# Kernel tuning notes

Measured on AMD Instinct MI355X. Metric: run time of the kernel, lower is better.

## Reference

```python
import jax, jax.numpy as jnp
import numpy as np


def setup_inputs() -> dict:
    key = jax.random.key(0)
    k1, k2 = jax.random.split(key)
    B, C, H, W = 8, 128, 96, 160
    x1 = jax.random.normal(k1, (B, C, H, W), dtype=jnp.float32)
    x2 = jax.random.normal(k2, (B, C, H, W), dtype=jnp.float32)
    return {"x1": x1, "x2": x2, "d": 4}


def reference(x1, x2, d):
    # x1, x2: (B, C, H, W); output: (B, (2d+1)^2, H, W)
    b, c, h, w = x1.shape
    x2p = jnp.pad(x2, ((0, 0), (0, 0), (d, d), (d, d)))
    # Loop over the small fixed (2d+1)^2 displacement set (81 for d=4);
    # each term is a channel-reduced elementwise product (shift-multiply-sum).
    corrs = [
        jnp.einsum("bchw,bchw->bhw", x1,
                   jax.lax.dynamic_slice(x2p, (0, 0, i, j), (b, c, h, w)))
        for i in range(2 * d + 1)
        for j in range(2 * d + 1)
    ]
    out = jnp.stack(corrs, axis=1)  # (B, (2d+1)^2, H, W)
    return out / c
```

## Files before the change

### kernel.cpp

```cpp
#include <hip/hip_runtime.h>
#include <stdint.h>
#include <stddef.h>

#define Bb 8
#define Cc 128
#define Hh 96
#define Ww 160
#define HW (Hh*Ww)
#define Kk 81

typedef __attribute__((ext_vector_type(8))) short short8;
typedef __attribute__((ext_vector_type(4))) float floatx4;
typedef __attribute__((ext_vector_type(4))) unsigned int uintx4;

__device__ __forceinline__ uint32_t bf16rne(float f) {
  uint32_t u = __float_as_uint(f);
  return (u + 0x7FFFu + ((u >> 16) & 1u)) >> 16;
}


#define TPX 32
__global__ __launch_bounds__(256)
void transpose_kernel(const float* __restrict__ x1, const float* __restrict__ x2,
                      ushort* __restrict__ x1t, ushort* __restrict__ x2t) {
  __shared__ float lds[TPX * 130];
  const int t   = threadIdx.x;
  const int b   = blockIdx.y;
  const int hw0 = blockIdx.x * TPX;
  const float* src = blockIdx.z ? x2 : x1;
  ushort*      dst = blockIdx.z ? x2t : x1t;

  const int p4 = t & 7;
  const int cb = t >> 3;
#pragma unroll
  for (int i = 0; i < 4; ++i) {
    const int c = cb + i * 32;
    floatx4 v = *(const floatx4*)&src[(size_t)(b * Cc + c) * HW + hw0 + p4 * 4];
#pragma unroll
    for (int jj = 0; jj < 4; ++jj)
      lds[(p4 * 4 + jj) * 130 + c] = v[jj];
  }
  __syncthreads();

  const int px = t >> 3;
#pragma unroll
  for (int i = 0; i < 2; ++i) {
    const int k = (t & 7) + 8 * i;
    const float* row = &lds[px * 130 + k * 8];
    uint32_t q0 = bf16rne(row[0]) | (bf16rne(row[1]) << 16);
    uint32_t q1 = bf16rne(row[2]) | (bf16rne(row[3]) << 16);
    uint32_t q2 = bf16rne(row[4]) | (bf16rne(row[5]) << 16);
    uint32_t q3 = bf16rne(row[6]) | (bf16rne(row[7]) << 16);
    *(uintx4*)&dst[((size_t)b * HW + hw0 + px) * Cc + k * 8] = (uintx4){q0, q1, q2, q3};
  }
}

#define LOADA(dst, tt, ckc)                                                    \
  {                                                                            \
    dst = (short8){0, 0, 0, 0, 0, 0, 0, 0};                                    \
    if (okw && (unsigned)(gh2b + (tt)) < (unsigned)Hh)                         \
      dst = *(const short8*)&base2[(long)(tt) * (Ww * Cc) + (ckc) * 32];       \
  }

__global__ __launch_bounds__(256, 3)
void corr_t2_kernel(const ushort* __restrict__ x1t, const ushort* __restrict__ x2t,
                    float* __restrict__ out) {
  const int tid  = threadIdx.x;
  const int flat = blockIdx.x;
  const int b  = flat & 7;
  const int j  = flat >> 3;
  const int by = j / 10;
  const int bx = j - by * 10;
  const int w0 = bx * 16;
  const int h0 = by * 4;

  const int lane = tid & 63;
  const int wv   = tid >> 6;
  const int vy = wv & 1, vx = wv >> 1;
  const int n = lane & 15, quad = lane >> 4;
  const int s = n >> 3, pw = n & 7;

  floatx4 acc[10];
#pragma unroll
  for (int t = 0; t < 10; ++t) acc[t] = (floatx4){0.f, 0.f, 0.f, 0.f};

  const int gw2  = w0 - 4 + 8 * vx + n;
  const bool okw = (unsigned)gw2 < (unsigned)Ww;
  const int gh2b = h0 - 4 + 2 * vy;
  const ushort* base2 = x2t + ((long)b * HW + (long)gh2b * Ww + gw2) * Cc + quad * 8;
  const ushort* base1 = x1t + ((long)b * HW + (long)(h0 + 2 * vy + s) * Ww
                               + (w0 + 8 * vx + pw)) * Cc + quad * 8;

  const short8 bf0 = *(const short8*)&base1[0 * 32];
  const short8 bf1 = *(const short8*)&base1[1 * 32];
  const short8 bf2 = *(const short8*)&base1[2 * 32];
  const short8 bf3 = *(const short8*)&base1[3 * 32];

  short8 aA0, aA1, aA2, aA3, aA4, aA5, aA6, aA7, aA8, aA9;
  short8 aB0, aB1, aB2, aB3, aB4, aB5, aB6, aB7, aB8, aB9;

  LOADA(aA0, 0, 0); LOADA(aA1, 1, 0); LOADA(aA2, 2, 0); LOADA(aA3, 3, 0);
  LOADA(aA4, 4, 0); LOADA(aA5, 5, 0); LOADA(aA6, 6, 0); LOADA(aA7, 7, 0);
  LOADA(aA8, 8, 0); LOADA(aA9, 9, 0);

  LOADA(aB0, 0, 1); LOADA(aB1, 1, 1); LOADA(aB2, 2, 1); LOADA(aB3, 3, 1);
  LOADA(aB4, 4, 1); LOADA(aB5, 5, 1); LOADA(aB6, 6, 1); LOADA(aB7, 7, 1);
  LOADA(aB8, 8, 1); LOADA(aB9, 9, 1);
  acc[0] = __builtin_amdgcn_mfma_f32_16x16x32_bf16(aA0, bf0, acc[0], 0, 0, 0);
  acc[1] = __builtin_amdgcn_mfma_f32_16x16x32_bf16(aA1, bf0, acc[1], 0, 0, 0);
  acc[2] = __builtin_amdgcn_mfma_f32_16x16x32_bf16(aA2, bf0, acc[2], 0, 0, 0);
  acc[3] = __builtin_amdgcn_mfma_f32_16x16x32_bf16(aA3, bf0, acc[3], 0, 0, 0);
  acc[4] = __builtin_amdgcn_mfma_f32_16x16x32_bf16(aA4, bf0, acc[4], 0, 0, 0);
  acc[5] = __builtin_amdgcn_mfma_f32_16x16x32_bf16(aA5, bf0, acc[5], 0, 0, 0);
  acc[6] = __builtin_amdgcn_mfma_f32_16x16x32_bf16(aA6, bf0, acc[6], 0, 0, 0);
  acc[7] = __builtin_amdgcn_mfma_f32_16x16x32_bf16(aA7, bf0, acc[7], 0, 0, 0);
  acc[8] = __builtin_amdgcn_mfma_f32_16x16x32_bf16(aA8, bf0, acc[8], 0, 0, 0);
  acc[9] = __builtin_amdgcn_mfma_f32_16x16x32_bf16(aA9, bf0, acc[9], 0, 0, 0);

  LOADA(aA0, 0, 2); LOADA(aA1, 1, 2); LOADA(aA2, 2, 2); LOADA(aA3, 3, 2);
  LOADA(aA4, 4, 2); LOADA(aA5, 5, 2); LOADA(aA6, 6, 2); LOADA(aA7, 7, 2);
  LOADA(aA8, 8, 2); LOADA(aA9, 9, 2);
  acc[0] = __builtin_amdgcn_mfma_f32_16x16x32_bf16(aB0, bf1, acc[0], 0, 0, 0);
  acc[1] = __builtin_amdgcn_mfma_f32_16x16x32_bf16(aB1, bf1, acc[1], 0, 0, 0);
  acc[2] = __builtin_amdgcn_mfma_f32_16x16x32_bf16(aB2, bf1, acc[2], 0, 0, 0);
  acc[3] = __builtin_amdgcn_mfma_f32_16x16x32_bf16(aB3, bf1, acc[3], 0, 0, 0);
  acc[4] = __builtin_amdgcn_mfma_f32_16x16x32_bf16(aB4, bf1, acc[4], 0, 0, 0);
  acc[5] = __builtin_amdgcn_mfma_f32_16x16x32_bf16(aB5, bf1, acc[5], 0, 0, 0);
  acc[6] = __builtin_amdgcn_mfma_f32_16x16x32_bf16(aB6, bf1, acc[6], 0, 0, 0);
  acc[7] = __builtin_amdgcn_mfma_f32_16x16x32_bf16(aB7, bf1, acc[7], 0, 0, 0);
  acc[8] = __builtin_amdgcn_mfma_f32_16x16x32_bf16(aB8, bf1, acc[8], 0, 0, 0);
  acc[9] = __builtin_amdgcn_mfma_f32_16x16x32_bf16(aB9, bf1, acc[9], 0, 0, 0);

  LOADA(aB0, 0, 3); LOADA(aB1, 1, 3); LOADA(aB2, 2, 3); LOADA(aB3, 3, 3);
  LOADA(aB4, 4, 3); LOADA(aB5, 5, 3); LOADA(aB6, 6, 3); LOADA(aB7, 7, 3);
  LOADA(aB8, 8, 3); LOADA(aB9, 9, 3);
  acc[0] = __builtin_amdgcn_mfma_f32_16x16x32_bf16(aA0, bf2, acc[0], 0, 0, 0);
  acc[1] = __builtin_amdgcn_mfma_f32_16x16x32_bf16(aA1, bf2, acc[1], 0, 0, 0);
  acc[2] = __builtin_amdgcn_mfma_f32_16x16x32_bf16(aA2, bf2, acc[2], 0, 0, 0);
  acc[3] = __builtin_amdgcn_mfma_f32_16x16x32_bf16(aA3, bf2, acc[3], 0, 0, 0);
  acc[4] = __builtin_amdgcn_mfma_f32_16x16x32_bf16(aA4, bf2, acc[4], 0, 0, 0);
  acc[5] = __builtin_amdgcn_mfma_f32_16x16x32_bf16(aA5, bf2, acc[5], 0, 0, 0);
  acc[6] = __builtin_amdgcn_mfma_f32_16x16x32_bf16(aA6, bf2, acc[6], 0, 0, 0);
  acc[7] = __builtin_amdgcn_mfma_f32_16x16x32_bf16(aA7, bf2, acc[7], 0, 0, 0);
  acc[8] = __builtin_amdgcn_mfma_f32_16x16x32_bf16(aA8, bf2, acc[8], 0, 0, 0);
  acc[9] = __builtin_amdgcn_mfma_f32_16x16x32_bf16(aA9, bf2, acc[9], 0, 0, 0);

  acc[0] = __builtin_amdgcn_mfma_f32_16x16x32_bf16(aB0, bf3, acc[0], 0, 0, 0);
  acc[1] = __builtin_amdgcn_mfma_f32_16x16x32_bf16(aB1, bf3, acc[1], 0, 0, 0);
  acc[2] = __builtin_amdgcn_mfma_f32_16x16x32_bf16(aB2, bf3, acc[2], 0, 0, 0);
  acc[3] = __builtin_amdgcn_mfma_f32_16x16x32_bf16(aB3, bf3, acc[3], 0, 0, 0);
  acc[4] = __builtin_amdgcn_mfma_f32_16x16x32_bf16(aB4, bf3, acc[4], 0, 0, 0);
  acc[5] = __builtin_amdgcn_mfma_f32_16x16x32_bf16(aB5, bf3, acc[5], 0, 0, 0);
  acc[6] = __builtin_amdgcn_mfma_f32_16x16x32_bf16(aB6, bf3, acc[6], 0, 0, 0);
  acc[7] = __builtin_amdgcn_mfma_f32_16x16x32_bf16(aB7, bf3, acc[7], 0, 0, 0);
  acc[8] = __builtin_amdgcn_mfma_f32_16x16x32_bf16(aB8, bf3, acc[8], 0, 0, 0);
  acc[9] = __builtin_amdgcn_mfma_f32_16x16x32_bf16(aB9, bf3, acc[9], 0, 0, 0);

  const float scale = 1.0f / 128.0f;
  const int ph  = h0 + 2 * vy + s;
  const int pwg = w0 + 8 * vx + pw;
#pragma unroll
  for (int t = 0; t < 10; ++t) {
    int di = t - 4 - s;
    if ((unsigned)(di + 4) > 8u) continue;
#pragma unroll
    for (int r = 0; r < 4; ++r) {
      int dj = quad * 4 + r - 4 - pw;
      if ((unsigned)(dj + 4) > 8u) continue;
      int kk = (di + 4) * 9 + (dj + 4);
      out[((size_t)b * Kk + kk) * HW + ph * Ww + pwg] = acc[t][r] * scale;
    }
  }
}

__global__ __launch_bounds__(512, 4)
void corr_kernel(const float* __restrict__ x1, const float* __restrict__ x2,
                 float* __restrict__ out) {
  __shared__ __align__(16) ushort ldsX2[16*24*40];
  __shared__ __align__(16) ushort ldsX1[8*16*40];

  const int tid = threadIdx.x;
  const int flat = blockIdx.x;
  const int b  = flat & 7;
  const int j  = flat >> 3;
  const int by = j / 10;
  const int bx = j - by * 10;
  const int w0 = bx * 16;
  const int h0 = by * 8;

  const int lane = tid & 63;
  const int wv   = tid >> 6;
  const int vy = wv & 3, vx = wv >> 2;
  const int n = lane & 15, quad = lane >> 4;
  const int s = n >> 3, pw = n & 7;

  floatx4 acc[10];
#pragma unroll
  for (int t = 0; t < 10; ++t) acc[t] = (floatx4){0.f, 0.f, 0.f, 0.f};

  for (int ck = 0; ck < 4; ++ck) {
    const int c0 = ck * 32;
    if (ck) __syncthreads();

#pragma unroll
    for (int it = 0; it < 3; ++it) {
      int T   = it * 512 + tid;
      int w24 = T % 24;
      int t2  = T / 24;
      int rw  = t2 & 15;
      int cg  = t2 >> 4;
      int gh = h0 - 4 + rw;
      int gw = w0 - 4 + w24;
      bool ok = ((unsigned)gh < Hh) && ((unsigned)gw < Ww);
      const float* src = x2 + ((size_t)(b*Cc + c0 + cg*8) * HW + gh*Ww + gw);
      uint32_t p0, p1, p2, p3;
      {
        float a0 = ok ? src[0*HW] : 0.f;
        float a1 = ok ? src[1*HW] : 0.f;
        float a2 = ok ? src[2*HW] : 0.f;
        float a3 = ok ? src[3*HW] : 0.f;
        float a4 = ok ? src[4*HW] : 0.f;
        float a5 = ok ? src[5*HW] : 0.f;
        float a6 = ok ? src[6*HW] : 0.f;
        float a7 = ok ? src[7*HW] : 0.f;
        p0 = bf16rne(a0) | (bf16rne(a1) << 16);
        p1 = bf16rne(a2) | (bf16rne(a3) << 16);
        p2 = bf16rne(a4) | (bf16rne(a5) << 16);
        p3 = bf16rne(a6) | (bf16rne(a7) << 16);
      }
      *(uintx4*)&ldsX2[(rw*24 + w24)*40 + cg*8] = (uintx4){p0, p1, p2, p3};
    }

    {
      int T  = tid;
      int wl = T & 15;
      int t2 = T >> 4;
      int rl = t2 & 7;
      int cg = t2 >> 3;
      const float* src = x1 + ((size_t)(b*Cc + c0 + cg*8) * HW
                               + (h0 + rl)*Ww + (w0 + wl));
      uint32_t p0, p1, p2, p3;
      float a0 = src[0*HW], a1 = src[1*HW], a2 = src[2*HW], a3 = src[3*HW];
      float a4 = src[4*HW], a5 = src[5*HW], a6 = src[6*HW], a7 = src[7*HW];
      p0 = bf16rne(a0) | (bf16rne(a1) << 16);
      p1 = bf16rne(a2) | (bf16rne(a3) << 16);
      p2 = bf16rne(a4) | (bf16rne(a5) << 16);
      p3 = bf16rne(a6) | (bf16rne(a7) << 16);
      *(uintx4*)&ldsX1[(rl*16 + wl)*40 + cg*8] = (uintx4){p0, p1, p2, p3};
    }

    __syncthreads();

    short8 bfrag = *(const short8*)&ldsX1[((2*vy + s)*16 + 8*vx + pw)*40 + quad*8];
#pragma unroll
    for (int t = 0; t < 10; ++t) {
      short8 afrag = *(const short8*)&ldsX2[((2*vy + t)*24 + 8*vx + n)*40 + quad*8];
      acc[t] = __builtin_amdgcn_mfma_f32_16x16x32_bf16(afrag, bfrag, acc[t], 0, 0, 0);
    }
  }

  const float scale = 1.0f / 128.0f;
  const int ph  = h0 + 2*vy + s;
  const int pwg = w0 + 8*vx + pw;
#pragma unroll
  for (int t = 0; t < 10; ++t) {
    int di = t - 4 - s;
    if ((unsigned)(di + 4) > 8u) continue;
#pragma unroll
    for (int r = 0; r < 4; ++r) {
      int dj = quad*4 + r - 4 - pw;
      if ((unsigned)(dj + 4) > 8u) continue;
      int kk = (di + 4) * 9 + (dj + 4);
      out[((size_t)b*Kk + kk) * HW + ph*Ww + pwg] = acc[t][r] * scale;
    }
  }
}

extern "C" void kernel_launch(void* const* d_in, const int* in_sizes, int n_in,
                              void* d_out, int out_size, void* d_ws, size_t ws_size,
                              hipStream_t stream) {
  const float* x1 = (const float*)d_in[0];
  const float* x2 = (const float*)d_in[1];
  float* out = (float*)d_out;

  const size_t elems = (size_t)Bb * HW * Cc;
  const size_t need  = 2 * elems * sizeof(ushort);

  if (d_ws != nullptr && ws_size >= need) {
    ushort* x1t = (ushort*)d_ws;
    ushort* x2t = x1t + elems;
    transpose_kernel<<<dim3(HW / TPX, Bb, 2), dim3(256, 1, 1), 0, stream>>>(
        x1, x2, x1t, x2t);
    corr_t2_kernel<<<dim3(1920, 1, 1), dim3(256, 1, 1), 0, stream>>>(x1t, x2t, out);
  } else {
    corr_kernel<<<dim3(960, 1, 1), dim3(512, 1, 1), 0, stream>>>(x1, x2, out);
  }
}
```

Baseline: 215.0 us.

## Make x2 loads unconditional with clamped rows and stage output through LDS

Result: faster. 207.0 us (-3.7%).

```diff
diff --git a/kernel.cpp b/kernel.cpp
--- a/kernel.cpp
+++ b/kernel.cpp
@@ -55,16 +55,24 @@
   }
 }
 
-#define LOADA(dst, tt, ckc)                                                    \
-  {                                                                            \
-    dst = (short8){0, 0, 0, 0, 0, 0, 0, 0};                                    \
-    if (okw && (unsigned)(gh2b + (tt)) < (unsigned)Hh)                         \
-      dst = *(const short8*)&base2[(long)(tt) * (Ww * Cc) + (ckc) * 32];       \
-  }
+__device__ __forceinline__ int clampi(int v, int lo, int hi) {
+  return v < lo ? lo : (v > hi ? hi : v);
+}
+
+#define LOADRAW(dst, tt, ckc)                                                  \
+  dst = *(const short8*)&base2c[rowoff##tt + (ckc) * 32];
+
+#define ZSEL(v, tt)                                                            \
+  v = (okw && (unsigned)(gh2b + (tt)) < (unsigned)Hh) ? v                      \
+      : (short8){0, 0, 0, 0, 0, 0, 0, 0};
+
+#define SBAR() __builtin_amdgcn_sched_barrier(0)
 
 __global__ __launch_bounds__(256, 3)
-void corr_t2_kernel(const ushort* __restrict__ x1t, const ushort* __restrict__ x2t,
+void corr_t3_kernel(const ushort* __restrict__ x1t, const ushort* __restrict__ x2t,
                     float* __restrict__ out) {
+  __shared__ float ldsOut[Kk * 66];
+
   const int tid  = threadIdx.x;
   const int flat = blockIdx.x;
   const int b  = flat & 7;
@@ -86,10 +94,23 @@
 
   const int gw2  = w0 - 4 + 8 * vx + n;
   const bool okw = (unsigned)gw2 < (unsigned)Ww;
+  const int gw2c = clampi(gw2, 0, Ww - 1);
   const int gh2b = h0 - 4 + 2 * vy;
-  const ushort* base2 = x2t + ((long)b * HW + (long)gh2b * Ww + gw2) * Cc + quad * 8;
-  const ushort* base1 = x1t + ((long)b * HW + (long)(h0 + 2 * vy + s) * Ww
-                               + (w0 + 8 * vx + pw)) * Cc + quad * 8;
+
+  const ushort* base2c = x2t + ((long)b * HW + gw2c) * Cc + quad * 8;
+  const ushort* base1  = x1t + ((long)b * HW + (long)(h0 + 2 * vy + s) * Ww
+                                + (w0 + 8 * vx + pw)) * Cc + quad * 8;
+
+  const long rowoff0 = (long)clampi(gh2b + 0, 0, Hh - 1) * (Ww * Cc);
+  const long rowoff1 = (long)clampi(gh2b + 1, 0, Hh - 1) * (Ww * Cc);
+  const long rowoff2 = (long)clampi(gh2b + 2, 0, Hh - 1) * (Ww * Cc);
+  const long rowoff3 = (long)clampi(gh2b + 3, 0, Hh - 1) * (Ww * Cc);
+  const long rowoff4 = (long)clampi(gh2b + 4, 0, Hh - 1) * (Ww * Cc);
+  const long rowoff5 = (long)clampi(gh2b + 5, 0, Hh - 1) * (Ww * Cc);
+  const long rowoff6 = (long)clampi(gh2b + 6, 0, Hh - 1) * (Ww * Cc);
+  const long rowoff7 = (long)clampi(gh2b + 7, 0, Hh - 1) * (Ww * Cc);
+  const long rowoff8 = (long)clampi(gh2b + 8, 0, Hh - 1) * (Ww * Cc);
+  const long rowoff9 = (long)clampi(gh2b + 9, 0, Hh - 1) * (Ww * Cc);
 
   const short8 bf0 = *(const short8*)&base1[0 * 32];
   const short8 bf1 = *(const short8*)&base1[1 * 32];
@@ -99,13 +120,16 @@
   short8 aA0, aA1, aA2, aA3, aA4, aA5, aA6, aA7, aA8, aA9;
   short8 aB0, aB1, aB2, aB3, aB4, aB5, aB6, aB7, aB8, aB9;
 
-  LOADA(aA0, 0, 0); LOADA(aA1, 1, 0); LOADA(aA2, 2, 0); LOADA(aA3, 3, 0);
-  LOADA(aA4, 4, 0); LOADA(aA5, 5, 0); LOADA(aA6, 6, 0); LOADA(aA7, 7, 0);
-  LOADA(aA8, 8, 0); LOADA(aA9, 9, 0);
-
-  LOADA(aB0, 0, 1); LOADA(aB1, 1, 1); LOADA(aB2, 2, 1); LOADA(aB3, 3, 1);
-  LOADA(aB4, 4, 1); LOADA(aB5, 5, 1); LOADA(aB6, 6, 1); LOADA(aB7, 7, 1);
-  LOADA(aB8, 8, 1); LOADA(aB9, 9, 1);
+  LOADRAW(aA0, 0, 0); LOADRAW(aA1, 1, 0); LOADRAW(aA2, 2, 0); LOADRAW(aA3, 3, 0);
+  LOADRAW(aA4, 4, 0); LOADRAW(aA5, 5, 0); LOADRAW(aA6, 6, 0); LOADRAW(aA7, 7, 0);
+  LOADRAW(aA8, 8, 0); LOADRAW(aA9, 9, 0);
+  SBAR();
+  LOADRAW(aB0, 0, 1); LOADRAW(aB1, 1, 1); LOADRAW(aB2, 2, 1); LOADRAW(aB3, 3, 1);
+  LOADRAW(aB4, 4, 1); LOADRAW(aB5, 5, 1); LOADRAW(aB6, 6, 1); LOADRAW(aB7, 7, 1);
+  LOADRAW(aB8, 8, 1); LOADRAW(aB9, 9, 1);
+  SBAR();
+  ZSEL(aA0, 0); ZSEL(aA1, 1); ZSEL(aA2, 2); ZSEL(aA3, 3); ZSEL(aA4, 4);
+  ZSEL(aA5, 5); ZSEL(aA6, 6); ZSEL(aA7, 7); ZSEL(aA8, 8); ZSEL(aA9, 9);
   acc[0] = __builtin_amdgcn_mfma_f32_16x16x32_bf16(aA0, bf0, acc[0], 0, 0, 0);
   acc[1] = __builtin_amdgcn_mfma_f32_16x16x32_bf16(aA1, bf0, acc[1], 0, 0, 0);
   acc[2] = __builtin_amdgcn_mfma_f32_16x16x32_bf16(aA2, bf0, acc[2], 0, 0, 0);
@@ -116,10 +140,13 @@
   acc[7] = __builtin_amdgcn_mfma_f32_16x16x32_bf16(aA7, bf0, acc[7], 0, 0, 0);
   acc[8] = __builtin_amdgcn_mfma_f32_16x16x32_bf16(aA8, bf0, acc[8], 0, 0, 0);
   acc[9] = __builtin_amdgcn_mfma_f32_16x16x32_bf16(aA9, bf0, acc[9], 0, 0, 0);
-
-  LOADA(aA0, 0, 2); LOADA(aA1, 1, 2); LOADA(aA2, 2, 2); LOADA(aA3, 3, 2);
-  LOADA(aA4, 4, 2); LOADA(aA5, 5, 2); LOADA(aA6, 6, 2); LOADA(aA7, 7, 2);
-  LOADA(aA8, 8, 2); LOADA(aA9, 9, 2);
+  SBAR();
+  LOADRAW(aA0, 0, 2); LOADRAW(aA1, 1, 2); LOADRAW(aA2, 2, 2); LOADRAW(aA3, 3, 2);
+  LOADRAW(aA4, 4, 2); LOADRAW(aA5, 5, 2); LOADRAW(aA6, 6, 2); LOADRAW(aA7, 7, 2);
+  LOADRAW(aA8, 8, 2); LOADRAW(aA9, 9, 2);
+  SBAR();
+  ZSEL(aB0, 0); ZSEL(aB1, 1); ZSEL(aB2, 2); ZSEL(aB3, 3); ZSEL(aB4, 4);
+  ZSEL(aB5, 5); ZSEL(aB6, 6); ZSEL(aB7, 7); ZSEL(aB8, 8); ZSEL(aB9, 9);
   acc[0] = __builtin_amdgcn_mfma_f32_16x16x32_bf16(aB0, bf1, acc[0], 0, 0, 0);
   acc[1] = __builtin_amdgcn_mfma_f32_16x16x32_bf16(aB1, bf1, acc[1], 0, 0, 0);
   acc[2] = __builtin_amdgcn_mfma_f32_16x16x32_bf16(aB2, bf1, acc[2], 0, 0, 0);
@@ -130,10 +157,13 @@
   acc[7] = __builtin_amdgcn_mfma_f32_16x16x32_bf16(aB7, bf1, acc[7], 0, 0, 0);
   acc[8] = __builtin_amdgcn_mfma_f32_16x16x32_bf16(aB8, bf1, acc[8], 0, 0, 0);
   acc[9] = __builtin_amdgcn_mfma_f32_16x16x32_bf16(aB9, bf1, acc[9], 0, 0, 0);
-
-  LOADA(aB0, 0, 3); LOADA(aB1, 1, 3); LOADA(aB2, 2, 3); LOADA(aB3, 3, 3);
-  LOADA(aB4, 4, 3); LOADA(aB5, 5, 3); LOADA(aB6, 6, 3); LOADA(aB7, 7, 3);
-  LOADA(aB8, 8, 3); LOADA(aB9, 9, 3);
+  SBAR();
+  LOADRAW(aB0, 0, 3); LOADRAW(aB1, 1, 3); LOADRAW(aB2, 2, 3); LOADRAW(aB3, 3, 3);
+  LOADRAW(aB4, 4, 3); LOADRAW(aB5, 5, 3); LOADRAW(aB6, 6, 3); LOADRAW(aB7, 7, 3);
+  LOADRAW(aB8, 8, 3); LOADRAW(aB9, 9, 3);
+  SBAR();
+  ZSEL(aA0, 0); ZSEL(aA1, 1); ZSEL(aA2, 2); ZSEL(aA3, 3); ZSEL(aA4, 4);
+  ZSEL(aA5, 5); ZSEL(aA6, 6); ZSEL(aA7, 7); ZSEL(aA8, 8); ZSEL(aA9, 9);
   acc[0] = __builtin_amdgcn_mfma_f32_16x16x32_bf16(aA0, bf2, acc[0], 0, 0, 0);
   acc[1] = __builtin_amdgcn_mfma_f32_16x16x32_bf16(aA1, bf2, acc[1], 0, 0, 0);
   acc[2] = __builtin_amdgcn_mfma_f32_16x16x32_bf16(aA2, bf2, acc[2], 0, 0, 0);
@@ -144,7 +174,9 @@
   acc[7] = __builtin_amdgcn_mfma_f32_16x16x32_bf16(aA7, bf2, acc[7], 0, 0, 0);
   acc[8] = __builtin_amdgcn_mfma_f32_16x16x32_bf16(aA8, bf2, acc[8], 0, 0, 0);
   acc[9] = __builtin_amdgcn_mfma_f32_16x16x32_bf16(aA9, bf2, acc[9], 0, 0, 0);
-
+  SBAR();
+  ZSEL(aB0, 0); ZSEL(aB1, 1); ZSEL(aB2, 2); ZSEL(aB3, 3); ZSEL(aB4, 4);
+  ZSEL(aB5, 5); ZSEL(aB6, 6); ZSEL(aB7, 7); ZSEL(aB8, 8); ZSEL(aB9, 9);
   acc[0] = __builtin_amdgcn_mfma_f32_16x16x32_bf16(aB0, bf3, acc[0], 0, 0, 0);
   acc[1] = __builtin_amdgcn_mfma_f32_16x16x32_bf16(aB1, bf3, acc[1], 0, 0, 0);
   acc[2] = __builtin_amdgcn_mfma_f32_16x16x32_bf16(aB2, bf3, acc[2], 0, 0, 0);
@@ -157,8 +189,8 @@
   acc[9] = __builtin_amdgcn_mfma_f32_16x16x32_bf16(aB9, bf3, acc[9], 0, 0, 0);
 
   const float scale = 1.0f / 128.0f;
-  const int ph  = h0 + 2 * vy + s;
-  const int pwg = w0 + 8 * vx + pw;
+  const int prow = 2 * vy + s;
+  const int pcol = 8 * vx + pw;
 #pragma unroll
   for (int t = 0; t < 10; ++t) {
     int di = t - 4 - s;
@@ -168,8 +200,18 @@
       int dj = quad * 4 + r - 4 - pw;
       if ((unsigned)(dj + 4) > 8u) continue;
       int kk = (di + 4) * 9 + (dj + 4);
-      out[((size_t)b * Kk + kk) * HW + ph * Ww + pwg] = acc[t][r] * scale;
-    }
+      ldsOut[kk * 66 + prow * 16 + pcol] = acc[t][r] * scale;
+    }
+  }
+  __syncthreads();
+
+  for (int idx = tid; idx < Kk * 64; idx += 256) {
+    int kk  = idx >> 6;
+    int rem = idx & 63;
+    int hh  = rem >> 4;
+    int ww  = rem & 15;
+    out[((size_t)b * Kk + kk) * HW + (size_t)(h0 + hh) * Ww + (w0 + ww)] =
+        ldsOut[kk * 66 + rem];
   }
 }
 
@@ -291,7 +333,7 @@
     ushort* x2t = x1t + elems;
     transpose_kernel<<<dim3(HW / TPX, Bb, 2), dim3(256, 1, 1), 0, stream>>>(
         x1, x2, x1t, x2t);
-    corr_t2_kernel<<<dim3(1920, 1, 1), dim3(256, 1, 1), 0, stream>>>(x1t, x2t, out);
+    corr_t3_kernel<<<dim3(1920, 1, 1), dim3(256, 1, 1), 0, stream>>>(x1t, x2t, out);
   } else {
     corr_kernel<<<dim3(960, 1, 1), dim3(512, 1, 1), 0, stream>>>(x1, x2, out);
   }
```
